# Performance work log

Hardware: AMD Instinct MI355X
Metric: run time of the kernel (lower is better)

The kernel has to match this reference:

```python
import jax, jax.numpy as jnp
import numpy as np

N, IN_DIM, H1, H2 = 12288, 512, 256, 128

def setup_inputs() -> dict:
    key = jax.random.key(0)
    k = jax.random.split(key, 6)
    glorot = lambda kk, fi, fo: jax.random.normal(kk, (fi, fo), jnp.float32) * np.sqrt(2.0 / (fi + fo))
    return {
        "X": jax.random.normal(k[0], (N, IN_DIM), jnp.float32),
        "adj": jax.random.uniform(k[1], (N, N), jnp.float32) / N,  # scaled like a normalized adjacency
        "noise": jax.random.normal(k[2], (N, H2), jnp.float32),
        "W0": glorot(k[3], IN_DIM, H1),
        "W_mu": glorot(k[4], H1, H2),
        "W_logstd": glorot(k[5], H1, H2),
    }

def reference(X, adj, noise, W0, W_mu, W_logstd):
    # GraphConvSparse layer 1: relu(adj @ (X @ W0))
    hidden = jax.nn.relu(adj @ (X @ W0))            # [N, H1]
    # mean / logstd heads (identity activation)
    mean = adj @ (hidden @ W_mu)                    # [N, H2]
    logstd = adj @ (hidden @ W_logstd)              # [N, H2]
    # reparameterization
    Z = noise * jnp.exp(logstd) + mean              # [N, H2]
    # dot-product decode
    A_pred = jax.nn.sigmoid(Z @ Z.T)                # [N, N]
    return A_pred
```

## Files before the change

kernel.cpp:

```cpp
#include <hip/hip_runtime.h>
#include <hip/hip_fp8.h>
#include <stdint.h>

#define NN 12288
#define IND 512
#define H1D 256
#define H2D 128

using bf16x8 = __attribute__((ext_vector_type(8))) short;
using f32x4  = __attribute__((ext_vector_type(4))) float;
using u32x4  = __attribute__((ext_vector_type(4))) unsigned int;

__device__ __forceinline__ unsigned short f2bf(float f){
  unsigned int u = __float_as_uint(f);
  return (unsigned short)((u + 0x7fffu + ((u >> 16) & 1u)) >> 16);
}
__device__ __forceinline__ float bf2f(unsigned short h){
  return __uint_as_float(((unsigned int)h) << 16);
}
__device__ __forceinline__ void gload_lds16(const void* g, void* l){
  __builtin_amdgcn_global_load_lds(
      (const __attribute__((address_space(1))) unsigned int*)(uintptr_t)g,
      (__attribute__((address_space(3))) unsigned int*)(unsigned int)(uintptr_t)l,
      16, 0, 0);
}
template<bool HI>
__device__ __forceinline__ unsigned cvt2(float a, float b, unsigned old){
#if __has_builtin(__builtin_amdgcn_cvt_pk_fp8_f32)
  return (unsigned)__builtin_amdgcn_cvt_pk_fp8_f32(a, b, (int)old, HI);
#else
  __hip_fp8_e4m3 pa(a), pb(b);
  unsigned v = (unsigned)pa.__x | ((unsigned)pb.__x << 8);
  return HI ? ((old & 0x0000FFFFu) | (v << 16)) : ((old & 0xFFFF0000u) | v);
#endif
}
__device__ __forceinline__ void sync0(){
  asm volatile("s_waitcnt vmcnt(0) lgkmcnt(0)" ::: "memory");
  __builtin_amdgcn_s_barrier();
  __builtin_amdgcn_sched_barrier(0);
}

__global__ __launch_bounds__(256) void k_cvt(const float* __restrict__ in,
                                             char* __restrict__ out,
                                             float scale, long n16){
  const long stride = (long)gridDim.x * 256;
  for (long i = (long)blockIdx.x * 256 + threadIdx.x; i < n16; i += stride){
    const f32x4* p = (const f32x4*)(in + i * 16);
    f32x4 a = __builtin_nontemporal_load(p);
    f32x4 b = __builtin_nontemporal_load(p + 1);
    f32x4 c = __builtin_nontemporal_load(p + 2);
    f32x4 d = __builtin_nontemporal_load(p + 3);
    u32x4 pk;
    pk[0] = cvt2<false>(a[0]*scale, a[1]*scale, 0u); pk[0] = cvt2<true>(a[2]*scale, a[3]*scale, pk[0]);
    pk[1] = cvt2<false>(b[0]*scale, b[1]*scale, 0u); pk[1] = cvt2<true>(b[2]*scale, b[3]*scale, pk[1]);
    pk[2] = cvt2<false>(c[0]*scale, c[1]*scale, 0u); pk[2] = cvt2<true>(c[2]*scale, c[3]*scale, pk[2]);
    pk[3] = cvt2<false>(d[0]*scale, d[1]*scale, 0u); pk[3] = cvt2<true>(d[2]*scale, d[3]*scale, pk[3]);
    *(u32x4*)(out + i * 16) = pk;
  }
}

__global__ __launch_bounds__(256) void k_w0t(const float* __restrict__ W0,
                                             char* __restrict__ W0T){
  __shared__ float Ls[64][65];
  const int t = (int)threadIdx.x;
  const int k0 = (int)blockIdx.x * 64;
  const int h0 = (int)blockIdx.y * 64;
  {
    const int r = t >> 2, c = (t & 3) * 16;
    const float* p = W0 + (size_t)(k0 + r) * H1D + h0 + c;
#pragma unroll
    for (int q = 0; q < 4; ++q)
      *(float4*)&Ls[r][c + q*4] = *(const float4*)(p + q*4);
  }
  __syncthreads();
  const int h = t >> 2, kc = (t & 3) * 16;
  u32x4 pk;
#pragma unroll
  for (int q = 0; q < 4; ++q){
    unsigned wv = cvt2<false>(Ls[kc+q*4+0][h], Ls[kc+q*4+1][h], 0u);
    wv = cvt2<true>(Ls[kc+q*4+2][h], Ls[kc+q*4+3][h], wv);
    pk[q] = wv;
  }
  *(u32x4*)(W0T + (size_t)(h0 + h) * IND + k0 + kc) = pk;
}

#define STAGE(BUF, SIDX) { \
  _Pragma("unroll") \
  for (int p = 0; p < 2; ++p) \
    gload_lds16(Ap + (size_t)(p*32) * lda + (size_t)(SIDX)*128, \
                Alds[BUF] + p*4096 + w*1024); \
  _Pragma("unroll") \
  for (int i = 0; i < 4; ++i) \
    gload_lds16(Bp + (size_t)(i*32) * ldb + (size_t)(SIDX)*128, \
                Blds[BUF] + i*4096 + w*1024); \
}

#define MF8(CUR) { \
  _Pragma("unroll") \
  for (int kk = 0; kk < 4; ++kk){ \
    long af[4]; long bfr[2]; \
    _Pragma("unroll") \
    for (int mi = 0; mi < 4; ++mi){ \
      int row = mi*16 + l15; \
      int off = row*128 + ((kk*32 + l16*8) ^ ((row & 7) << 4)); \
      af[mi] = *(const long*)(Alds[CUR] + off); \
    } \
    _Pragma("unroll") \
    for (int ni = 0; ni < 2; ++ni){ \
      int row = w*32 + ni*16 + l15; \
      int off = row*128 + ((kk*32 + l16*8) ^ ((row & 7) << 4)); \
      bfr[ni] = *(const long*)(Blds[CUR] + off); \
    } \
    _Pragma("unroll") \
    for (int mi = 0; mi < 4; ++mi) \
      _Pragma("unroll") \
      for (int ni = 0; ni < 2; ++ni) \
        acc[mi][ni] = __builtin_amdgcn_mfma_f32_16x16x32_fp8_fp8(af[mi], bfr[ni], acc[mi][ni], 0, 0, 0); \
  } }

template<int KSPLIT, int MODE>
__global__ __launch_bounds__(256, 3) void k_gf8(const char* __restrict__ A, int lda, int K,
                                                const char* __restrict__ Bt, int ldb,
                                                void* __restrict__ Out){
  __shared__ __align__(16) char Alds[2][64*128];
  __shared__ __align__(16) char Blds[2][128*128];
  const int t = (int)threadIdx.x;
  const int w = t >> 6, l = t & 63;
  const int l15 = l & 15, l16 = l >> 4;

  int khalf, idx;
  if (KSPLIT == 2){
    int f = (int)blockIdx.x, x = f & 7;
    khalf = x >> 2;
    idx = (f >> 3) * 4 + (x & 3);
  } else { khalf = 0; idx = (int)blockIdx.x; }
  const int m0 = (idx >> 1) * 64;
  const int nh = idx & 1;
  const size_t kb = (size_t)khalf * K;
  const int S = K >> 7;

  f32x4 acc[4][2];
#pragma unroll
  for (int mi = 0; mi < 4; ++mi)
#pragma unroll
    for (int ni = 0; ni < 2; ++ni) acc[mi][ni] = 0;

  const int swz = ((l & 7) ^ (l >> 3)) << 4;
  const char* Ap = A  + (size_t)(m0 + w*8 + (l >> 3)) * lda + kb + swz;
  const char* Bp = Bt + (size_t)(nh*128 + w*8 + (l >> 3)) * ldb + kb + swz;

  STAGE(0, 0);
  sync0();
  for (int s = 0; s < S; ++s){
    const int cur = s & 1;
    if (s + 1 < S){ if (cur == 0){ STAGE(1, s + 1); } else { STAGE(0, s + 1); } }
    if (cur == 0){ MF8(0); } else { MF8(1); }
    if (s + 1 < S) sync0();
  }

  if (MODE == 0){
    char* OutT = (char*)Out;
#pragma unroll
    for (int mi = 0; mi < 4; ++mi)
#pragma unroll
      for (int ni = 0; ni < 2; ++ni){
        int gr = m0 + mi*16 + l16*4;
        int gc = nh*128 + w*32 + ni*16 + l15;
        unsigned wd = cvt2<false>(acc[mi][ni][0], acc[mi][ni][1], 0u);
        wd = cvt2<true>(acc[mi][ni][2], acc[mi][ni][3], wd);
        *(unsigned*)(OutT + (size_t)gc * NN + gr) = wd;
      }
  } else {
    float* P = (float*)Out + (size_t)khalf * NN * H1D;
#pragma unroll
    for (int mi = 0; mi < 4; ++mi)
#pragma unroll
      for (int ni = 0; ni < 2; ++ni){
        int gr = m0 + mi*16 + l16*4;
        int gc = nh*128 + w*32 + ni*16 + l15;
#pragma unroll
        for (int v = 0; v < 4; ++v)
          P[(size_t)(gr + v) * H1D + gc] = acc[mi][ni][v];
      }
  }
}

__global__ __launch_bounds__(256) void k_combine_ht(const float* __restrict__ p0,
                                                    const float* __restrict__ p1,
                                                    char* __restrict__ HT){
  __shared__ float Ls[64][65];
  const int t = (int)threadIdx.x;
  const int n0 = (int)blockIdx.x * 64;
  const int h0 = (int)blockIdx.y * 64;
  const int lr = t >> 4, lc = (t & 15) * 4;
#pragma unroll
  for (int q = 0; q < 4; ++q){
    int n = lr + q*16;
    size_t idx = (size_t)(n0 + n) * H1D + h0 + lc;
    float4 a = *(const float4*)(p0 + idx);
    float4 b = *(const float4*)(p1 + idx);
    Ls[n][lc+0] = fmaxf(a.x + b.x, 0.f);
    Ls[n][lc+1] = fmaxf(a.y + b.y, 0.f);
    Ls[n][lc+2] = fmaxf(a.z + b.z, 0.f);
    Ls[n][lc+3] = fmaxf(a.w + b.w, 0.f);
  }
  __syncthreads();
  const int hr = t >> 2, nc = (t & 3) * 16;
  u32x4 pk;
#pragma unroll
  for (int q = 0; q < 4; ++q){
    unsigned wd = cvt2<false>(Ls[nc+q*4+0][hr], Ls[nc+q*4+1][hr], 0u);
    wd = cvt2<true>(Ls[nc+q*4+2][hr], Ls[nc+q*4+3][hr], wd);
    pk[q] = wd;
  }
  *(u32x4*)(HT + (size_t)(h0 + hr) * NN + n0 + nc) = pk;
}

__global__ __launch_bounds__(256) void k_heads(const float* __restrict__ p0,
                                               const float* __restrict__ Wmu,
                                               const float* __restrict__ Wls,
                                               const float* __restrict__ noise,
                                               unsigned short* __restrict__ Zhi,
                                               unsigned short* __restrict__ Zlo){
  __shared__ float AHs[32][256];
  __shared__ float Wms[32][128];
  __shared__ float Wlss[32][128];
  const float INV = 1.0f / 67108864.0f;
  const float* p1 = p0 + (size_t)NN * H1D;
  const int t  = (int)threadIdx.x;
  const int r0 = (int)blockIdx.x * 32;
  {
    const int r = t >> 3, c0 = (t & 7) * 32;
    size_t base = (size_t)(r0 + r) * H1D + c0;
#pragma unroll
    for (int q = 0; q < 8; ++q){
      float4 a = *(const float4*)(p0 + base + q*4);
      float4 b = *(const float4*)(p1 + base + q*4);
      AHs[r][c0 + q*4 + 0] = (a.x + b.x) * INV;
      AHs[r][c0 + q*4 + 1] = (a.y + b.y) * INV;
      AHs[r][c0 + q*4 + 2] = (a.z + b.z) * INV;
      AHs[r][c0 + q*4 + 3] = (a.w + b.w) * INV;
    }
  }
  const int j = t & 127, rg = t >> 7;
  float mu[16], ls[16];
#pragma unroll
  for (int r = 0; r < 16; ++r){ mu[r] = 0.f; ls[r] = 0.f; }

  for (int kc = 0; kc < 8; ++kc){
    __syncthreads();
    {
      const int r = t >> 3, c0 = (t & 7) * 16;
      const float* pm = Wmu + (size_t)(kc*32 + r) * H2D + c0;
      const float* pl = Wls + (size_t)(kc*32 + r) * H2D + c0;
#pragma unroll
      for (int q = 0; q < 4; ++q){
        *(float4*)&Wms[r][c0 + q*4]  = *(const float4*)(pm + q*4);
        *(float4*)&Wlss[r][c0 + q*4] = *(const float4*)(pl + q*4);
      }
    }
    __syncthreads();
#pragma unroll 4
    for (int k = 0; k < 32; ++k){
      float wm = Wms[k][j], wl = Wlss[k][j];
#pragma unroll
      for (int r = 0; r < 16; ++r){
        float a = AHs[rg*16 + r][kc*32 + k];
        mu[r] += a * wm;
        ls[r] += a * wl;
      }
    }
  }
#pragma unroll
  for (int r = 0; r < 16; ++r){
    const int i = r0 + rg*16 + r;
    float z = noise[(size_t)i * H2D + j] * __expf(ls[r]) + mu[r];
    unsigned short zh = f2bf(z);
    unsigned short zl = f2bf(z - bf2f(zh));
    Zhi[(size_t)i * H2D + j] = zh;
    Zlo[(size_t)i * H2D + j] = zl;
  }
}

__global__ __launch_bounds__(512, 2) void k_decode(const unsigned short* __restrict__ Zhi,
                                                   const unsigned short* __restrict__ Zlo,
                                                   float* __restrict__ Out){
  __shared__ __align__(16) char SMEM[65536];
  unsigned short* T0 = (unsigned short*)SMEM;
  float (*Ls)[133] = (float(*)[133])SMEM;

  const int i = (int)blockIdx.x;
  int by = (int)((sqrtf(8.0f * (float)i + 1.0f) - 1.0f) * 0.5f);
  while ((by + 1) * (by + 2) / 2 <= i) ++by;
  while (by * (by + 1) / 2 > i) --by;
  const int bx = i - by * (by + 1) / 2;
  const bool diag = (bx == by);

  const int t = (int)threadIdx.x;
  const int w = t >> 6, l = t & 63;
  const int l15 = l & 15, l16 = l >> 4;
  const int wr = w >> 2, wc = w & 3;
  const size_t m0 = (size_t)bx * 128;
  const size_t n0 = (size_t)by * 128;

  f32x4 acc[4][2];
#pragma unroll
  for (int mi = 0; mi < 4; ++mi)
#pragma unroll
    for (int ni = 0; ni < 2; ++ni) acc[mi][ni] = 0;

#pragma unroll
  for (int p = 0; p < 2; ++p){
    if (p) __syncthreads();
#pragma unroll
    for (int i2 = 0; i2 < 2; ++i2){
      int P = i2*8192 + t*16;
      int row = P >> 7;
      int Li = (P & 127) ^ ((row & 7) << 4);
      size_t ga = (size_t)row * 256 + (size_t)p * 128 + Li;
      char* lb = (char*)T0 + i2*8192 + w*1024;
      gload_lds16((const char*)Zhi + m0*256 + ga, lb);
      gload_lds16((const char*)Zlo + m0*256 + ga, lb + 16384);
      gload_lds16((const char*)Zhi + n0*256 + ga, lb + 32768);
      gload_lds16((const char*)Zlo + n0*256 + ga, lb + 49152);
    }
    __syncthreads();
#pragma unroll
    for (int kk = 0; kk < 2; ++kk){
      bf16x8 ah[4], al[4], bh[2], bl[2];
#pragma unroll
      for (int mi = 0; mi < 4; ++mi){
        int row = wr*64 + mi*16 + l15;
        int off = row*128 + ((kk*64 + l16*16) ^ ((row & 7) << 4));
        ah[mi] = *(const bf16x8*)((const char*)T0 + off);
        al[mi] = *(const bf16x8*)((const char*)T0 + 16384 + off);
      }
#pragma unroll
      for (int ni = 0; ni < 2; ++ni){
        int row = wc*32 + ni*16 + l15;
        int off = row*128 + ((kk*64 + l16*16) ^ ((row & 7) << 4));
        bh[ni] = *(const bf16x8*)((const char*)T0 + 32768 + off);
        bl[ni] = *(const bf16x8*)((const char*)T0 + 49152 + off);
      }
#pragma unroll
      for (int mi = 0; mi < 4; ++mi)
#pragma unroll
        for (int ni = 0; ni < 2; ++ni){
          acc[mi][ni] = __builtin_amdgcn_mfma_f32_16x16x32_bf16(ah[mi], bh[ni], acc[mi][ni], 0, 0, 0);
          acc[mi][ni] = __builtin_amdgcn_mfma_f32_16x16x32_bf16(ah[mi], bl[ni], acc[mi][ni], 0, 0, 0);
          acc[mi][ni] = __builtin_amdgcn_mfma_f32_16x16x32_bf16(al[mi], bh[ni], acc[mi][ni], 0, 0, 0);
        }
    }
  }

#pragma unroll
  for (int p = 0; p < 2; ++p){
    __syncthreads();
    if (wr == p){
#pragma unroll
      for (int mi = 0; mi < 4; ++mi)
#pragma unroll
        for (int ni = 0; ni < 2; ++ni)
#pragma unroll
          for (int v = 0; v < 4; ++v){
            float sg = 1.0f / (1.0f + __expf(-acc[mi][ni][v]));
            Ls[mi*16 + l16*4 + v][wc*32 + ni*16 + l15] = sg;
          }
    }
    __syncthreads();
    {
      const int r = t >> 3, c0 = (t & 7) * 16;
      float* dst = &Out[(m0 + (size_t)(p*64 + r)) * NN + n0 + c0];
      const float* src = &Ls[r][c0];
#pragma unroll
      for (int q = 0; q < 4; ++q)
        *(f32x4*)(dst + q*4) = *(const f32x4*)(src + q*4);
    }
    if (!diag){
      const int a = t >> 2, b0 = (t & 3) * 16;
      float vv[16];
#pragma unroll
      for (int k = 0; k < 16; ++k) vv[k] = Ls[b0 + k][a];
      float* dst = &Out[(n0 + (size_t)a) * NN + m0 + (size_t)(p*64 + b0)];
#pragma unroll
      for (int q = 0; q < 4; ++q){
        f32x4 pk = { vv[q*4+0], vv[q*4+1], vv[q*4+2], vv[q*4+3] };
        *(f32x4*)(dst + q*4) = pk;
      }
    }
  }
}

extern "C" void kernel_launch(void* const* d_in, const int* in_sizes, int n_in,
                              void* d_out, int out_size, void* d_ws, size_t ws_size,
                              hipStream_t stream) {
  const float* X     = (const float*)d_in[0];
  const float* adj   = (const float*)d_in[1];
  const float* noise = (const float*)d_in[2];
  const float* W0    = (const float*)d_in[3];
  const float* Wmu   = (const float*)d_in[4];
  const float* Wls   = (const float*)d_in[5];
  float* out = (float*)d_out;
  char* ws = (char*)d_ws;

  char*           XW0Tf8 = ws;
  char*           HidTf8 = ws + 3145728;
  char*           W0Tf8  = ws + 6291456;
  unsigned short* Zhi    = (unsigned short*)(ws + 6422528);
  unsigned short* Zlo    = (unsigned short*)(ws + 9568256);
  char*           Xf8    = ws + 12713984;
  char*  adjf8 = (char*)d_out;
  float* part  = (float*)((char*)d_out + 150994944);

  const float S_ADJ = 8192.0f;

  k_cvt<<<2048, 256, 0, stream>>>(adj, adjf8, S_ADJ, (long)NN * NN / 16);
  k_w0t<<<dim3(8, 4), 256, 0, stream>>>(W0, W0Tf8);
  k_cvt<<<256, 256, 0, stream>>>(X, Xf8, 1.0f, (long)NN * IND / 16);
  k_gf8<1,0><<<384, 256, 0, stream>>>(Xf8, IND, IND, W0Tf8, IND, (void*)XW0Tf8);
  k_gf8<2,1><<<768, 256, 0, stream>>>(adjf8, NN, 6144, XW0Tf8, NN, (void*)part);
  k_combine_ht<<<dim3(192, 4), 256, 0, stream>>>(part, part + (size_t)NN * H1D, HidTf8);
  k_gf8<2,1><<<768, 256, 0, stream>>>(adjf8, NN, 6144, HidTf8, NN, (void*)part);
  k_heads<<<384, 256, 0, stream>>>(part, Wmu, Wls, noise, Zhi, Zlo);
  k_decode<<<4656, 512, 0, stream>>>(Zhi, Zlo, out);
}
```

Before: 605.5 us.

## Enlarge fp8 GEMM tiles to 128x128 with 512 threads and split-K of four

The fp8 adjacency GEMM now uses 512-thread blocks, each computing a 128x128 output tile with 8 waves in a 2x4 layout, in place of 64x128 tiles from 256 threads. This halves the number of times the B operand is reloaded per row of A. Split-K goes from 2 to 4 to keep the grid at 768 blocks, so the combine and heads kernels now sum four fp32 partial buffers, which adds partial-sum traffic. The decode kernel also remaps block indices into 8 interleaved strided groups, likely to improve cache locality or spread work across XCDs.

```diff
diff --git a/kernel.cpp b/kernel.cpp
--- a/kernel.cpp
+++ b/kernel.cpp
@@ -87,12 +87,12 @@
 #define STAGE(BUF, SIDX) { \
   _Pragma("unroll") \
   for (int p = 0; p < 2; ++p) \
-    gload_lds16(Ap + (size_t)(p*32) * lda + (size_t)(SIDX)*128, \
-                Alds[BUF] + p*4096 + w*1024); \
+    gload_lds16(Ap + (size_t)(p*8) * lda + (size_t)(SIDX)*128, \
+                Alds[BUF] + w*2048 + p*1024); \
   _Pragma("unroll") \
-  for (int i = 0; i < 4; ++i) \
-    gload_lds16(Bp + (size_t)(i*32) * ldb + (size_t)(SIDX)*128, \
-                Blds[BUF] + i*4096 + w*1024); \
+  for (int p = 0; p < 2; ++p) \
+    gload_lds16(Bp + (size_t)(p*8) * ldb + (size_t)(SIDX)*128, \
+                Blds[BUF] + w*2048 + p*1024); \
 }
 
 #define MF8(CUR) { \
@@ -101,13 +101,13 @@
     long af[4]; long bfr[2]; \
     _Pragma("unroll") \
     for (int mi = 0; mi < 4; ++mi){ \
-      int row = mi*16 + l15; \
+      int row = wr*64 + mi*16 + l15; \
       int off = row*128 + ((kk*32 + l16*8) ^ ((row & 7) << 4)); \
       af[mi] = *(const long*)(Alds[CUR] + off); \
     } \
     _Pragma("unroll") \
     for (int ni = 0; ni < 2; ++ni){ \
-      int row = w*32 + ni*16 + l15; \
+      int row = wc*32 + ni*16 + l15; \
       int off = row*128 + ((kk*32 + l16*8) ^ ((row & 7) << 4)); \
       bfr[ni] = *(const long*)(Blds[CUR] + off); \
     } \
@@ -119,23 +119,23 @@
   } }
 
 template<int KSPLIT, int MODE>
-__global__ __launch_bounds__(256, 3) void k_gf8(const char* __restrict__ A, int lda, int K,
+__global__ __launch_bounds__(512, 4) void k_gf8(const char* __restrict__ A, int lda, int K,
                                                 const char* __restrict__ Bt, int ldb,
                                                 void* __restrict__ Out){
-  __shared__ __align__(16) char Alds[2][64*128];
+  __shared__ __align__(16) char Alds[2][128*128];
   __shared__ __align__(16) char Blds[2][128*128];
   const int t = (int)threadIdx.x;
   const int w = t >> 6, l = t & 63;
   const int l15 = l & 15, l16 = l >> 4;
-
-  int khalf, idx;
-  if (KSPLIT == 2){
+  const int wr = w >> 2, wc = w & 3;
+
+  int khalf, nh, m0;
+  if (KSPLIT == 4){
     int f = (int)blockIdx.x, x = f & 7;
-    khalf = x >> 2;
-    idx = (f >> 3) * 4 + (x & 3);
-  } else { khalf = 0; idx = (int)blockIdx.x; }
-  const int m0 = (idx >> 1) * 64;
-  const int nh = idx & 1;
+    khalf = x >> 1; nh = x & 1; m0 = (f >> 3) * 128;
+  } else {
+    khalf = 0; nh = (int)blockIdx.x & 1; m0 = ((int)blockIdx.x >> 1) * 128;
+  }
   const size_t kb = (size_t)khalf * K;
   const int S = K >> 7;
 
@@ -146,8 +146,8 @@
     for (int ni = 0; ni < 2; ++ni) acc[mi][ni] = 0;
 
   const int swz = ((l & 7) ^ (l >> 3)) << 4;
-  const char* Ap = A  + (size_t)(m0 + w*8 + (l >> 3)) * lda + kb + swz;
-  const char* Bp = Bt + (size_t)(nh*128 + w*8 + (l >> 3)) * ldb + kb + swz;
+  const char* Ap = A  + (size_t)(m0 + w*16 + (l >> 3)) * lda + kb + swz;
+  const char* Bp = Bt + (size_t)(nh*128 + w*16 + (l >> 3)) * ldb + kb + swz;
 
   STAGE(0, 0);
   sync0();
@@ -164,8 +164,8 @@
     for (int mi = 0; mi < 4; ++mi)
 #pragma unroll
       for (int ni = 0; ni < 2; ++ni){
-        int gr = m0 + mi*16 + l16*4;
-        int gc = nh*128 + w*32 + ni*16 + l15;
+        int gr = m0 + wr*64 + mi*16 + l16*4;
+        int gc = nh*128 + wc*32 + ni*16 + l15;
         unsigned wd = cvt2<false>(acc[mi][ni][0], acc[mi][ni][1], 0u);
         wd = cvt2<true>(acc[mi][ni][2], acc[mi][ni][3], wd);
         *(unsigned*)(OutT + (size_t)gc * NN + gr) = wd;
@@ -176,8 +176,8 @@
     for (int mi = 0; mi < 4; ++mi)
 #pragma unroll
       for (int ni = 0; ni < 2; ++ni){
-        int gr = m0 + mi*16 + l16*4;
-        int gc = nh*128 + w*32 + ni*16 + l15;
+        int gr = m0 + wr*64 + mi*16 + l16*4;
+        int gc = nh*128 + wc*32 + ni*16 + l15;
 #pragma unroll
         for (int v = 0; v < 4; ++v)
           P[(size_t)(gr + v) * H1D + gc] = acc[mi][ni][v];
@@ -186,9 +186,9 @@
 }
 
 __global__ __launch_bounds__(256) void k_combine_ht(const float* __restrict__ p0,
-                                                    const float* __restrict__ p1,
                                                     char* __restrict__ HT){
   __shared__ float Ls[64][65];
+  const size_t PS = (size_t)NN * H1D;
   const int t = (int)threadIdx.x;
   const int n0 = (int)blockIdx.x * 64;
   const int h0 = (int)blockIdx.y * 64;
@@ -198,11 +198,13 @@
     int n = lr + q*16;
     size_t idx = (size_t)(n0 + n) * H1D + h0 + lc;
     float4 a = *(const float4*)(p0 + idx);
-    float4 b = *(const float4*)(p1 + idx);
-    Ls[n][lc+0] = fmaxf(a.x + b.x, 0.f);
-    Ls[n][lc+1] = fmaxf(a.y + b.y, 0.f);
-    Ls[n][lc+2] = fmaxf(a.z + b.z, 0.f);
-    Ls[n][lc+3] = fmaxf(a.w + b.w, 0.f);
+    float4 b = *(const float4*)(p0 + PS + idx);
+    float4 c = *(const float4*)(p0 + 2*PS + idx);
+    float4 d = *(const float4*)(p0 + 3*PS + idx);
+    Ls[n][lc+0] = fmaxf(a.x + b.x + c.x + d.x, 0.f);
+    Ls[n][lc+1] = fmaxf(a.y + b.y + c.y + d.y, 0.f);
+    Ls[n][lc+2] = fmaxf(a.z + b.z + c.z + d.z, 0.f);
+    Ls[n][lc+3] = fmaxf(a.w + b.w + c.w + d.w, 0.f);
   }
   __syncthreads();
   const int hr = t >> 2, nc = (t & 3) * 16;
@@ -226,7 +228,7 @@
   __shared__ float Wms[32][128];
   __shared__ float Wlss[32][128];
   const float INV = 1.0f / 67108864.0f;
-  const float* p1 = p0 + (size_t)NN * H1D;
+  const size_t PS = (size_t)NN * H1D;
   const int t  = (int)threadIdx.x;
   const int r0 = (int)blockIdx.x * 32;
   {
@@ -235,11 +237,13 @@
 #pragma unroll
     for (int q = 0; q < 8; ++q){
       float4 a = *(const float4*)(p0 + base + q*4);
-      float4 b = *(const float4*)(p1 + base + q*4);
-      AHs[r][c0 + q*4 + 0] = (a.x + b.x) * INV;
-      AHs[r][c0 + q*4 + 1] = (a.y + b.y) * INV;
-      AHs[r][c0 + q*4 + 2] = (a.z + b.z) * INV;
-      AHs[r][c0 + q*4 + 3] = (a.w + b.w) * INV;
+      float4 b = *(const float4*)(p0 + PS + base + q*4);
+      float4 c = *(const float4*)(p0 + 2*PS + base + q*4);
+      float4 d = *(const float4*)(p0 + 3*PS + base + q*4);
+      AHs[r][c0 + q*4 + 0] = (a.x + b.x + c.x + d.x) * INV;
+      AHs[r][c0 + q*4 + 1] = (a.y + b.y + c.y + d.y) * INV;
+      AHs[r][c0 + q*4 + 2] = (a.z + b.z + c.z + d.z) * INV;
+      AHs[r][c0 + q*4 + 3] = (a.w + b.w + c.w + d.w) * INV;
     }
   }
   const int j = t & 127, rg = t >> 7;
@@ -289,7 +293,8 @@
   unsigned short* T0 = (unsigned short*)SMEM;
   float (*Ls)[133] = (float(*)[133])SMEM;
 
-  const int i = (int)blockIdx.x;
+  const int b = (int)blockIdx.x;
+  const int i = (b & 7) * 582 + (b >> 3);
   int by = (int)((sqrtf(8.0f * (float)i + 1.0f) - 1.0f) * 0.5f);
   while ((by + 1) * (by + 2) / 2 <= i) ++by;
   while (by * (by + 1) / 2 > i) --by;
@@ -417,10 +422,10 @@
   k_cvt<<<2048, 256, 0, stream>>>(adj, adjf8, S_ADJ, (long)NN * NN / 16);
   k_w0t<<<dim3(8, 4), 256, 0, stream>>>(W0, W0Tf8);
   k_cvt<<<256, 256, 0, stream>>>(X, Xf8, 1.0f, (long)NN * IND / 16);
-  k_gf8<1,0><<<384, 256, 0, stream>>>(Xf8, IND, IND, W0Tf8, IND, (void*)XW0Tf8);
-  k_gf8<2,1><<<768, 256, 0, stream>>>(adjf8, NN, 6144, XW0Tf8, NN, (void*)part);
-  k_combine_ht<<<dim3(192, 4), 256, 0, stream>>>(part, part + (size_t)NN * H1D, HidTf8);
-  k_gf8<2,1><<<768, 256, 0, stream>>>(adjf8, NN, 6144, HidTf8, NN, (void*)part);
+  k_gf8<1,0><<<192, 512, 0, stream>>>(Xf8, IND, IND, W0Tf8, IND, (void*)XW0Tf8);
+  k_gf8<4,1><<<768, 512, 0, stream>>>(adjf8, NN, 3072, XW0Tf8, NN, (void*)part);
+  k_combine_ht<<<dim3(192, 4), 256, 0, stream>>>(part, HidTf8);
+  k_gf8<4,1><<<768, 512, 0, stream>>>(adjf8, NN, 3072, HidTf8, NN, (void*)part);
   k_heads<<<384, 256, 0, stream>>>(part, Wmu, Wls, noise, Zhi, Zlo);
   k_decode<<<4656, 512, 0, stream>>>(Zhi, Zlo, out);
 }
```

Result: slower. 636.5 us (+5.1%).

## Fuse adjacency fp32-to-fp8 conversion into first adj GEMM

Applied to the files above, without the earlier changes.

Removes the standalone conversion pass over the fp32 adjacency and instead has the first adj×XW0 GEMM load fp32 adj tiles directly. It converts them to fp8 in registers, writes them to LDS for the MFMA, and also dumps the fp8 copy to global for the second GEMM. The goal is to save one full extra read of the fp32 adjacency and a separate kernel launch. The cost is higher register pressure and per-iteration conversion work in the GEMM's critical loop, with the A operand now going through registers instead of direct global-to-LDS loads.

```diff
diff --git a/kernel.cpp b/kernel.cpp
--- a/kernel.cpp
+++ b/kernel.cpp
@@ -36,6 +36,11 @@
 }
 __device__ __forceinline__ void sync0(){
   asm volatile("s_waitcnt vmcnt(0) lgkmcnt(0)" ::: "memory");
+  __builtin_amdgcn_s_barrier();
+  __builtin_amdgcn_sched_barrier(0);
+}
+__device__ __forceinline__ void sync2(){
+  asm volatile("s_waitcnt vmcnt(2) lgkmcnt(0)" ::: "memory");
   __builtin_amdgcn_s_barrier();
   __builtin_amdgcn_sched_barrier(0);
 }
@@ -185,6 +190,100 @@
   }
 }
 
+#define FSTAGE_B(BUF, SIDX) { \
+  _Pragma("unroll") \
+  for (int i = 0; i < 4; ++i) \
+    gload_lds16(Bp + (size_t)(i*32) * ldb + (size_t)(SIDX)*128, \
+                Blds[BUF] + i*4096 + w*1024); \
+}
+
+#define FLOADA(SIDX) { \
+  const f32x4* p = (const f32x4*)(Af + (size_t)(SIDX)*128); \
+  _Pragma("unroll") \
+  for (int q = 0; q < 8; ++q) r[q] = __builtin_nontemporal_load(p + q); \
+}
+
+#define FPACKA(BUF, SIDX) { \
+  u32x4 pk0, pk1; \
+  pk0[0] = cvt2<false>(r[0][0]*ascale, r[0][1]*ascale, 0u); pk0[0] = cvt2<true>(r[0][2]*ascale, r[0][3]*ascale, pk0[0]); \
+  pk0[1] = cvt2<false>(r[1][0]*ascale, r[1][1]*ascale, 0u); pk0[1] = cvt2<true>(r[1][2]*ascale, r[1][3]*ascale, pk0[1]); \
+  pk0[2] = cvt2<false>(r[2][0]*ascale, r[2][1]*ascale, 0u); pk0[2] = cvt2<true>(r[2][2]*ascale, r[2][3]*ascale, pk0[2]); \
+  pk0[3] = cvt2<false>(r[3][0]*ascale, r[3][1]*ascale, 0u); pk0[3] = cvt2<true>(r[3][2]*ascale, r[3][3]*ascale, pk0[3]); \
+  pk1[0] = cvt2<false>(r[4][0]*ascale, r[4][1]*ascale, 0u); pk1[0] = cvt2<true>(r[4][2]*ascale, r[4][3]*ascale, pk1[0]); \
+  pk1[1] = cvt2<false>(r[5][0]*ascale, r[5][1]*ascale, 0u); pk1[1] = cvt2<true>(r[5][2]*ascale, r[5][3]*ascale, pk1[1]); \
+  pk1[2] = cvt2<false>(r[6][0]*ascale, r[6][1]*ascale, 0u); pk1[2] = cvt2<true>(r[6][2]*ascale, r[6][3]*ascale, pk1[2]); \
+  pk1[3] = cvt2<false>(r[7][0]*ascale, r[7][1]*ascale, 0u); pk1[3] = cvt2<true>(r[7][2]*ascale, r[7][3]*ascale, pk1[3]); \
+  *(u32x4*)(Alds[BUF] + aoff0) = pk0; \
+  *(u32x4*)(Alds[BUF] + aoff1) = pk1; \
+  *(u32x4*)(dmp + (size_t)(SIDX)*128)      = pk0; \
+  *(u32x4*)(dmp + (size_t)(SIDX)*128 + 16) = pk1; \
+}
+
+__global__ __launch_bounds__(256, 3) void k_gf8_acvt(const float* __restrict__ A, int K,
+                                                     const char* __restrict__ Bt, int ldb,
+                                                     float ascale, char* __restrict__ dump,
+                                                     float* __restrict__ Out){
+  __shared__ __align__(16) char Alds[2][64*128];
+  __shared__ __align__(16) char Blds[2][128*128];
+  const int t = (int)threadIdx.x;
+  const int w = t >> 6, l = t & 63;
+  const int l15 = l & 15, l16 = l >> 4;
+
+  int f = (int)blockIdx.x, x = f & 7;
+  const int khalf = x >> 2;
+  const int idx = (f >> 3) * 4 + (x & 3);
+  const int m0 = (idx >> 1) * 64;
+  const int nh = idx & 1;
+  const size_t kb = (size_t)khalf * K;
+  const int S = K >> 7;
+
+  f32x4 acc[4][2];
+#pragma unroll
+  for (int mi = 0; mi < 4; ++mi)
+#pragma unroll
+    for (int ni = 0; ni < 2; ++ni) acc[mi][ni] = 0;
+
+  const int swz = ((l & 7) ^ (l >> 3)) << 4;
+  const char* Bp = Bt + (size_t)(nh*128 + w*8 + (l >> 3)) * ldb + kb + swz;
+  const int ar = t >> 2, ac = (t & 3) * 32;
+  const float* Af = A + (size_t)(m0 + ar) * NN + kb + ac;
+  const int aoff0 = ar*128 + ( ac       ^ ((ar & 7) << 4));
+  const int aoff1 = ar*128 + ((ac + 16) ^ ((ar & 7) << 4));
+  char* dmp = dump + (size_t)(m0 + ar) * NN + kb + ac;
+  f32x4 r[8];
+
+  FSTAGE_B(0, 0);
+  __builtin_amdgcn_sched_barrier(0);
+  FLOADA(0);
+  FPACKA(0, 0);
+  sync2();
+  for (int s = 0; s < S; ++s){
+    const int cur = s & 1, nxt = cur ^ 1;
+    if (s + 1 < S){
+      if (cur == 0){ FSTAGE_B(1, s + 1); } else { FSTAGE_B(0, s + 1); }
+      __builtin_amdgcn_sched_barrier(0);
+      FLOADA(s + 1);
+    }
+    if (cur == 0){ MF8(0); } else { MF8(1); }
+    if (s + 1 < S){
+      if (cur == 0){ FPACKA(1, s + 1); } else { FPACKA(0, s + 1); }
+      sync2();
+    }
+  }
+
+  float* P = Out + (size_t)khalf * NN * H1D;
+#pragma unroll
+  for (int mi = 0; mi < 4; ++mi)
+#pragma unroll
+    for (int ni = 0; ni < 2; ++ni){
+      int gr = m0 + mi*16 + l16*4;
+      int gc = nh*128 + w*32 + ni*16 + l15;
+#pragma unroll
+      for (int v = 0; v < 4; ++v)
+        P[(size_t)(gr + v) * H1D + gc] = acc[mi][ni][v];
+    }
+}
+
 __global__ __launch_bounds__(256) void k_combine_ht(const float* __restrict__ p0,
                                                     const float* __restrict__ p1,
                                                     char* __restrict__ HT){
@@ -414,11 +513,10 @@
 
   const float S_ADJ = 8192.0f;
 
-  k_cvt<<<2048, 256, 0, stream>>>(adj, adjf8, S_ADJ, (long)NN * NN / 16);
   k_w0t<<<dim3(8, 4), 256, 0, stream>>>(W0, W0Tf8);
   k_cvt<<<256, 256, 0, stream>>>(X, Xf8, 1.0f, (long)NN * IND / 16);
   k_gf8<1,0><<<384, 256, 0, stream>>>(Xf8, IND, IND, W0Tf8, IND, (void*)XW0Tf8);
-  k_gf8<2,1><<<768, 256, 0, stream>>>(adjf8, NN, 6144, XW0Tf8, NN, (void*)part);
+  k_gf8_acvt<<<768, 256, 0, stream>>>(adj, 6144, XW0Tf8, NN, S_ADJ, adjf8, part);
   k_combine_ht<<<dim3(192, 4), 256, 0, stream>>>(part, part + (size_t)NN * H1D, HidTf8);
   k_gf8<2,1><<<768, 256, 0, stream>>>(adjf8, NN, 6144, HidTf8, NN, (void*)part);
   k_heads<<<384, 256, 0, stream>>>(part, Wmu, Wls, noise, Zhi, Zlo);
```

Result: slower. 1.096 ms (+81.0%).
